# Optimization experiments

Measured on AMD Instinct MI355X. Metric: run time of the kernel, lower is better.

The kernel has to match this reference:

```python
import jax, jax.numpy as jnp
import numpy as np

B, N, H, IN, OUT = 2, 4096, 64, 32, 8


def setup_inputs() -> dict:
    key = jax.random.key(0)
    ks = jax.random.split(key, 18)
    sc = 0.1  # xavier-ish scale for H=64
    mask = lambda k: (jax.random.uniform(k, (1, N, N)) < 0.1).astype(jnp.float32)
    return {
        "x0": jax.random.normal(ks[0], (B, N, IN), jnp.float32),
        "h0": jax.random.normal(ks[1], (B, N, H), jnp.float32),
        "h1": jax.random.normal(ks[2], (B, N, H), jnp.float32),
        "h2": jax.random.normal(ks[3], (B, N, H), jnp.float32),
        "m00": mask(ks[4]), "m20": mask(ks[5]), "m01": mask(ks[6]),
        "m11": mask(ks[7]), "m12": mask(ks[8]), "m22": mask(ks[9]),
        "Wq": jax.random.normal(ks[10], (3, H, H), jnp.float32) * sc,
        "Wk": jax.random.normal(ks[11], (6, H, H), jnp.float32) * sc,
        "Wsu0": jax.random.normal(ks[12], (H, IN + H), jnp.float32) * sc,
        "Wsu12": jax.random.normal(ks[13], (2, H, H), jnp.float32) * sc,
        "Wdt": jax.random.normal(ks[14], (3, H, H), jnp.float32) * sc,
        "bdt": jnp.zeros((3, H), jnp.float32),
        "step_size": jnp.array(1.0, jnp.float32),
        "out_scale": jnp.array(10.0, jnp.float32),
    }


def _cosine_acc(q, keys_and_masks_and_vals):
    # q: [B,N,H]; each entry: (keys [B,Np,H], mask [1,N,Np], vals [B,Np,H])
    qn = q / jnp.linalg.norm(q, axis=2, keepdims=True)
    acc = 0.0
    for k, m, v in keys_and_masks_and_vals:
        kn = k / jnp.linalg.norm(k, axis=2, keepdims=True)
        scale = 1.0 / jnp.sum(m, axis=2, keepdims=True)
        rel = scale * m * jnp.einsum("bnh,bmh->bnm", qn, kn)  # [B,N,Np]
        acc = acc + jnp.einsum("bnm,bmh->bnh", rel, v)
    return acc


def reference(x0, h0, h1, h2, m00, m20, m01, m11, m12, m22,
              Wq, Wk, Wsu0, Wsu12, Wdt, bdt, step_size, out_scale):
    # queries per successor type, keys per edge; edges (pred->succ):
    # 0->0 (k0), 2->0 (k1), 0->1 (k2), 1->1 (k3), 1->2 (k4), 2->2 (k5)
    q0 = h0 @ Wq[0].T
    q1 = h1 @ Wq[1].T
    q2 = h2 @ Wq[2].T
    acc0 = _cosine_acc(q0, [(h0 @ Wk[0].T, m00, h0), (h2 @ Wk[1].T, m20, h2)])
    acc1 = _cosine_acc(q1, [(h0 @ Wk[2].T, m01, h0), (h1 @ Wk[3].T, m11, h1)])
    acc2 = _cosine_acc(q2, [(h1 @ Wk[4].T, m12, h1), (h2 @ Wk[5].T, m22, h2)])

    def step(h, acc_in, Wsu, t):
        dt = 2.0 * jax.nn.sigmoid(h @ Wdt[t].T + bdt[t]) - 1.0
        return h + step_size * dt * (acc_in @ Wsu.T)

    h0n = step(h0, jnp.concatenate([x0, acc0], axis=2), Wsu0, 0)
    h1n = step(h1, acc1, Wsu12[0], 1)
    h2n = step(h2, acc2, Wsu12[1], 2)
    out2 = out_scale * h2n[:, :, :OUT]
    return (out2, h0n, h1n, h2n)
```

## Files before the change

### kernel.cpp

```cpp
#include <hip/hip_runtime.h>

typedef __bf16 bf16;
typedef bf16 bf16x8 __attribute__((ext_vector_type(8)));
typedef float f32x4 __attribute__((ext_vector_type(4)));
typedef unsigned int uint;
typedef uint u32x4 __attribute__((ext_vector_type(4)));
typedef unsigned short u16x8 __attribute__((ext_vector_type(8)));

constexpr int NT = 4096;

__device__ __forceinline__ bf16x8 ld8f(const float* p) {
    f32x4 a = *(const f32x4*)p;
    f32x4 b = *(const f32x4*)(p + 4);
    bf16x8 v;
    v[0] = (bf16)a[0]; v[1] = (bf16)a[1]; v[2] = (bf16)a[2]; v[3] = (bf16)a[3];
    v[4] = (bf16)b[0]; v[5] = (bf16)b[1]; v[6] = (bf16)b[2]; v[7] = (bf16)b[3];
    return v;
}

__device__ __forceinline__ uint pack2(float a, float b) {
    unsigned short ua = __builtin_bit_cast(unsigned short, (bf16)a);
    unsigned short ub = __builtin_bit_cast(unsigned short, (bf16)b);
    return (uint)ua | ((uint)ub << 16);
}

__global__ __launch_bounds__(256) void prep_kernel(
    const float* __restrict__ h0, const float* __restrict__ h1, const float* __restrict__ h2,
    const float* __restrict__ Wq, const float* __restrict__ Wk,
    bf16* __restrict__ qn, bf16* __restrict__ kn, bf16* __restrict__ vT)
{
    __shared__ __align__(16) unsigned short tlds[4][16][72];
    const int tid = threadIdx.x, wid = tid >> 6, lane = tid & 63;
    const int l15 = lane & 15, quad = lane >> 4;
    const int bx = blockIdx.x;
    const int rt = bx & 127, sl = bx >> 7;
    const int g0 = rt * 64;
    const int grow = g0 + wid * 16 + l15;
    const float* hs[3] = {h0, h1, h2};

    bf16x8 af[3][2];
#pragma unroll
    for (int p = 0; p < 3; p++)
#pragma unroll
        for (int hc = 0; hc < 2; hc++)
            af[p][hc] = ld8f(hs[p] + (size_t)grow * 64 + hc * 32 + quad * 8);

    if (sl == 0) {
        const int gr0 = g0 + wid * 16;
        const int bb = gr0 >> 12, n0 = gr0 & 4095;
#pragma unroll
        for (int p = 0; p < 3; p++) {
#pragma unroll
            for (int hc = 0; hc < 2; hc++)
                *(u16x8*)(&tlds[wid][l15][hc * 32 + quad * 8]) = __builtin_bit_cast(u16x8, af[p][hc]);
            unsigned short vals[16];
#pragma unroll
            for (int r = 0; r < 16; r++) vals[r] = tlds[wid][r][lane];
            uint us[8];
#pragma unroll
            for (int k = 0; k < 8; k++) us[k] = (uint)vals[2 * k] | ((uint)vals[2 * k + 1] << 16);
            uint* dst = (uint*)(vT + ((size_t)(p * 2 + bb) * 64 + lane) * NT + n0);
            u32x4 w0 = {us[0], us[1], us[2], us[3]};
            u32x4 w1 = {us[4], us[5], us[6], us[7]};
            *(u32x4*)dst = w0;
            *(u32x4*)(dst + 4) = w1;
        }
    }

    const int predmap[6] = {0, 2, 0, 1, 1, 2};
    const int pj0 = sl * 3;
#pragma unroll
    for (int pi = 0; pi < 3; pi++) {
        const int pj = pj0 + pi;
        const float* W = (pj < 3) ? (Wq + pj * 4096) : (Wk + (pj - 3) * 4096);
        const int src = (pj < 3) ? pj : predmap[pj - 3];
        bf16* outp = (pj < 3) ? (qn + (size_t)pj * 2 * NT * 64)
                              : (kn + (size_t)(pj - 3) * 2 * NT * 64);
        f32x4 s[4];
#pragma unroll
        for (int it = 0; it < 4; it++) {
            f32x4 acc = {0.f, 0.f, 0.f, 0.f};
#pragma unroll
            for (int hc = 0; hc < 2; hc++) {
                bf16x8 wb = ld8f(W + (size_t)(it * 16 + l15) * 64 + hc * 32 + quad * 8);
                acc = __builtin_amdgcn_mfma_f32_16x16x32_bf16(af[src][hc], wb, acc, 0, 0, 0);
            }
            s[it] = acc;
        }
#pragma unroll
        for (int r = 0; r < 4; r++) {
            float ss = s[0][r] * s[0][r] + s[1][r] * s[1][r] + s[2][r] * s[2][r] + s[3][r] * s[3][r];
            ss += __shfl_xor(ss, 1); ss += __shfl_xor(ss, 2);
            ss += __shfl_xor(ss, 4); ss += __shfl_xor(ss, 8);
            float rn = rsqrtf(ss);
            s[0][r] *= rn; s[1][r] *= rn; s[2][r] *= rn; s[3][r] *= rn;
        }
        const int rowbase = g0 + wid * 16 + quad * 4;
#pragma unroll
        for (int it = 0; it < 4; it++)
#pragma unroll
            for (int r = 0; r < 4; r++)
                outp[(size_t)(rowbase + r) * 64 + it * 16 + l15] = (bf16)s[it][r];
    }
}

template<int JC>
__global__ __launch_bounds__(256, 3) void attn_kernel(
    const bf16* __restrict__ qn, const bf16* __restrict__ kn, const bf16* __restrict__ vT,
    const float* __restrict__ m00, const float* __restrict__ m20, const float* __restrict__ m01,
    const float* __restrict__ m11, const float* __restrict__ m12, const float* __restrict__ m22,
    float* __restrict__ Pacc, float* __restrict__ rsO)
{
    __shared__ __align__(16) bf16 Klds[2][64][72];
    __shared__ __align__(16) bf16 Vlds[2][64][72];
    const int tid = threadIdx.x, wid = tid >> 6, lane = tid & 63;
    const int l15 = lane & 15, quad = lane >> 4;
    const int bx = blockIdx.x;
    const int e = bx / (32 * JC);
    const int rem = bx % (32 * JC);
    const int qt = rem / JC, jcv = rem % JC;
    const int qrow0 = qt * 128, wstrip = wid * 32;
    const int qtypemap[6] = {0, 0, 1, 1, 2, 2};
    const int predmap[6]  = {0, 2, 0, 1, 1, 2};
    const float* masks[6] = {m00, m20, m01, m11, m12, m22};
    const float* __restrict__ mask = masks[e];
    const int qtv = qtypemap[e], pv = predmap[e];
    constexpr int JSPAN = NT / JC;
    constexpr int NI = JSPAN / 64;
    const int jbeg = jcv * JSPAN;

    int s_b[4], s_jl[4], s_ch[4];
#pragma unroll
    for (int i = 0; i < 4; i++) {
        int u = tid + 256 * i;
        s_b[i] = u >> 9; s_jl[i] = (u >> 3) & 63; s_ch[i] = u & 7;
    }

    bf16x8 Qf[2][2][2];
#pragma unroll
    for (int b = 0; b < 2; b++)
#pragma unroll
        for (int mt = 0; mt < 2; mt++)
#pragma unroll
            for (int hc = 0; hc < 2; hc++)
                Qf[b][mt][hc] = *(const bf16x8*)(qn +
                    ((size_t)(qtv * 2 + b) * NT + qrow0 + wstrip + mt * 16 + l15) * 64 +
                    hc * 32 + quad * 8);

    f32x4 acc2[2][4][2];
#pragma unroll
    for (int b = 0; b < 2; b++)
#pragma unroll
        for (int ht = 0; ht < 4; ht++)
#pragma unroll
            for (int mt = 0; mt < 2; mt++) {
                f32x4 z = {0.f, 0.f, 0.f, 0.f};
                acc2[b][ht][mt] = z;
            }
    float rsl[2] = {0.f, 0.f};

    u32x4 kreg[4], vreg[4];
#pragma unroll
    for (int i = 0; i < 4; i++) {
        kreg[i] = *(const u32x4*)(kn + ((size_t)(e * 2 + s_b[i]) * NT + jbeg + s_jl[i]) * 64 + s_ch[i] * 8);
        vreg[i] = *(const u32x4*)(vT + ((size_t)(pv * 2 + s_b[i]) * 64 + s_jl[i]) * NT + jbeg + s_ch[i] * 8);
    }
    f32x4 mv[2][4];
#pragma unroll
    for (int mt = 0; mt < 2; mt++)
#pragma unroll
        for (int jt = 0; jt < 4; jt++)
            mv[mt][jt] = *(const f32x4*)(mask +
                (size_t)(qrow0 + wstrip + mt * 16 + l15) * NT + jbeg + jt * 16 + quad * 4);

#pragma unroll 1
    for (int ji = 0; ji < NI; ji++) {
        const int jn = (ji + 1 < NI) ? (jbeg + (ji + 1) * 64) : jbeg;

        __syncthreads();
#pragma unroll
        for (int i = 0; i < 4; i++) {
            *(u32x4*)(&Klds[s_b[i]][s_jl[i]][s_ch[i] * 8]) = kreg[i];
            *(u32x4*)(&Vlds[s_b[i]][s_jl[i]][s_ch[i] * 8]) = vreg[i];
        }
        __syncthreads();

#pragma unroll
        for (int i = 0; i < 4; i++) {
            kreg[i] = *(const u32x4*)(kn + ((size_t)(e * 2 + s_b[i]) * NT + jn + s_jl[i]) * 64 + s_ch[i] * 8);
            vreg[i] = *(const u32x4*)(vT + ((size_t)(pv * 2 + s_b[i]) * 64 + s_jl[i]) * NT + jn + s_ch[i] * 8);
        }

#pragma unroll
        for (int mt = 0; mt < 2; mt++)
#pragma unroll
            for (int jt = 0; jt < 4; jt++)
                rsl[mt] += mv[mt][jt][0] + mv[mt][jt][1] + mv[mt][jt][2] + mv[mt][jt][3];

        uint Pd[2][4][2][2];
#pragma unroll
        for (int jt = 0; jt < 4; jt++)
#pragma unroll
            for (int b = 0; b < 2; b++)
#pragma unroll
                for (int mt = 0; mt < 2; mt++) {
                    f32x4 sc = {0.f, 0.f, 0.f, 0.f};
#pragma unroll
                    for (int hc = 0; hc < 2; hc++) {
                        bf16x8 a = *(const bf16x8*)(&Klds[b][jt * 16 + l15][hc * 32 + quad * 8]);
                        sc = __builtin_amdgcn_mfma_f32_16x16x32_bf16(a, Qf[b][mt][hc], sc, 0, 0, 0);
                    }
                    sc[0] *= mv[mt][jt][0]; sc[1] *= mv[mt][jt][1];
                    sc[2] *= mv[mt][jt][2]; sc[3] *= mv[mt][jt][3];
                    Pd[b][jt][mt][0] = pack2(sc[0], sc[1]);
                    Pd[b][jt][mt][1] = pack2(sc[2], sc[3]);
                }

#pragma unroll
        for (int mt = 0; mt < 2; mt++)
#pragma unroll
            for (int jt = 0; jt < 4; jt++)
                mv[mt][jt] = *(const f32x4*)(mask +
                    (size_t)(qrow0 + wstrip + mt * 16 + l15) * NT + jn + jt * 16 + quad * 4);

#pragma unroll
        for (int b = 0; b < 2; b++) {
            uint Bf[2][2][4];
#pragma unroll
            for (int mt = 0; mt < 2; mt++)
#pragma unroll
                for (int c = 0; c < 2; c++)
#pragma unroll
                    for (int v = 0; v < 4; v++) {
                        int srclane = ((((quad & 1) * 2 + (v >> 1)) * 16 + l15) << 2);
                        int lo = __builtin_amdgcn_ds_bpermute(srclane, (int)Pd[b][2 * c][mt][v & 1]);
                        int hi = __builtin_amdgcn_ds_bpermute(srclane, (int)Pd[b][2 * c + 1][mt][v & 1]);
                        Bf[mt][c][v] = (quad & 2) ? (uint)hi : (uint)lo;
                    }
#pragma unroll
            for (int ht = 0; ht < 4; ht++)
#pragma unroll
                for (int c = 0; c < 2; c++) {
                    bf16x8 a = *(const bf16x8*)(&Vlds[b][ht * 16 + l15][c * 32 + quad * 8]);
#pragma unroll
                    for (int mt = 0; mt < 2; mt++) {
                        u32x4 t = {Bf[mt][c][0], Bf[mt][c][1], Bf[mt][c][2], Bf[mt][c][3]};
                        bf16x8 bbv = __builtin_bit_cast(bf16x8, t);
                        acc2[b][ht][mt] =
                            __builtin_amdgcn_mfma_f32_16x16x32_bf16(a, bbv, acc2[b][ht][mt], 0, 0, 0);
                    }
                }
        }
    }

#pragma unroll
    for (int b = 0; b < 2; b++)
#pragma unroll
        for (int ht = 0; ht < 4; ht++)
#pragma unroll
            for (int mt = 0; mt < 2; mt++) {
                const int n = qrow0 + wstrip + mt * 16 + l15;
#pragma unroll
                for (int r = 0; r < 4; r++) {
                    const int h = ht * 16 + quad * 4 + r;
                    Pacc[(((size_t)(jcv * 6 + e) * 2 + b) * 64 + h) * NT + n] = acc2[b][ht][mt][r];
                }
            }
#pragma unroll
    for (int mt = 0; mt < 2; mt++) {
        float v = rsl[mt];
        v += __shfl_xor(v, 16);
        v += __shfl_xor(v, 32);
        if (quad == 0)
            rsO[(size_t)(jcv * 6 + e) * NT + qrow0 + wstrip + mt * 16 + l15] = v;
    }
}

template<int JC>
__global__ __launch_bounds__(256) void update_kernel(
    const float* __restrict__ x0, const float* __restrict__ h0,
    const float* __restrict__ h1, const float* __restrict__ h2,
    const float* __restrict__ Wsu0, const float* __restrict__ Wsu12,
    const float* __restrict__ Wdt, const float* __restrict__ bdt,
    const float* __restrict__ stepp, const float* __restrict__ oscp,
    const float* __restrict__ Pacc, const float* __restrict__ rs,
    float* __restrict__ dout)
{
    const int tid = threadIdx.x, wid = tid >> 6, lane = tid & 63;
    const int l15 = lane & 15, quad = lane >> 4;
    const int bx = blockIdx.x;
    const int rt = bx & 127, t = bx >> 7;
    const int g0 = rt * 64;
    const int grow = g0 + wid * 16 + l15;
    const int n = grow & 4095, bb = grow >> 12;
    const float step = *stepp, osc = *oscp;
    const float* hs[3] = {h0, h1, h2};
    const float* __restrict__ ht_base = hs[t];

    bf16x8 afh[2], afacc[2], afx;
#pragma unroll
    for (int hc = 0; hc < 2; hc++)
        afh[hc] = ld8f(ht_base + (size_t)grow * 64 + hc * 32 + quad * 8);
    if (t == 0) afx = ld8f(x0 + (size_t)grow * 32 + quad * 8);

    float s0 = 0.f, s1 = 0.f;
#pragma unroll
    for (int jc = 0; jc < JC; jc++) {
        s0 += rs[(size_t)(jc * 6 + 2 * t) * NT + n];
        s1 += rs[(size_t)(jc * 6 + 2 * t + 1) * NT + n];
    }
    const float i0 = 1.f / s0, i1 = 1.f / s1;
#pragma unroll
    for (int hc = 0; hc < 2; hc++) {
        float S0[8] = {0,0,0,0,0,0,0,0}, S1[8] = {0,0,0,0,0,0,0,0};
#pragma unroll
        for (int jc = 0; jc < JC; jc++) {
            const float* b0 = Pacc + (((size_t)(jc * 6 + 2 * t) * 2 + bb) * 64) * NT + n;
            const float* b1 = Pacc + (((size_t)(jc * 6 + 2 * t + 1) * 2 + bb) * 64) * NT + n;
#pragma unroll
            for (int j = 0; j < 8; j++) {
                const int h = hc * 32 + quad * 8 + j;
                S0[j] += b0[(size_t)h * NT];
                S1[j] += b1[(size_t)h * NT];
            }
        }
        bf16x8 v;
#pragma unroll
        for (int j = 0; j < 8; j++) v[j] = (bf16)(S0[j] * i0 + S1[j] * i1);
        afacc[hc] = v;
    }

    float bdtv[4];
#pragma unroll
    for (int it = 0; it < 4; it++)
        bdtv[it] = bdt[t * 64 + it * 16 + l15];

#pragma unroll
    for (int it = 0; it < 4; it++) {
        f32x4 z = {0.f, 0.f, 0.f, 0.f};
        f32x4 u = {0.f, 0.f, 0.f, 0.f};
#pragma unroll
        for (int hc = 0; hc < 2; hc++) {
            bf16x8 wb = ld8f(Wdt + (size_t)t * 4096 + (size_t)(it * 16 + l15) * 64 + hc * 32 + quad * 8);
            z = __builtin_amdgcn_mfma_f32_16x16x32_bf16(afh[hc], wb, z, 0, 0, 0);
        }
        if (t == 0) {
            bf16x8 w0 = ld8f(Wsu0 + (size_t)(it * 16 + l15) * 96 + quad * 8);
            u = __builtin_amdgcn_mfma_f32_16x16x32_bf16(afx, w0, u, 0, 0, 0);
#pragma unroll
            for (int kc = 0; kc < 2; kc++) {
                bf16x8 wk = ld8f(Wsu0 + (size_t)(it * 16 + l15) * 96 + 32 + kc * 32 + quad * 8);
                u = __builtin_amdgcn_mfma_f32_16x16x32_bf16(afacc[kc], wk, u, 0, 0, 0);
            }
        } else {
#pragma unroll
            for (int kc = 0; kc < 2; kc++) {
                bf16x8 wk = ld8f(Wsu12 + (size_t)(t - 1) * 4096 + (size_t)(it * 16 + l15) * 64 + kc * 32 + quad * 8);
                u = __builtin_amdgcn_mfma_f32_16x16x32_bf16(afacc[kc], wk, u, 0, 0, 0);
            }
        }
        const int colg = it * 16 + l15;
#pragma unroll
        for (int r = 0; r < 4; r++) {
            int row = g0 + wid * 16 + quad * 4 + r;
            float zz = z[r] + bdtv[it];
            float dtv = 2.f / (1.f + __expf(-zz)) - 1.f;
            float hval = ht_base[(size_t)row * 64 + colg];
            float hn = hval + step * dtv * u[r];
            dout[65536 + (size_t)t * 524288 + (size_t)row * 64 + colg] = hn;
            if (t == 2 && colg < 8)
                dout[(size_t)row * 8 + colg] = osc * hn;
        }
    }
}

extern "C" void kernel_launch(void* const* d_in, const int* in_sizes, int n_in,
                              void* d_out, int out_size, void* d_ws, size_t ws_size,
                              hipStream_t stream) {
    const float* x0   = (const float*)d_in[0];
    const float* h0   = (const float*)d_in[1];
    const float* h1   = (const float*)d_in[2];
    const float* h2   = (const float*)d_in[3];
    const float* m00  = (const float*)d_in[4];
    const float* m20  = (const float*)d_in[5];
    const float* m01  = (const float*)d_in[6];
    const float* m11  = (const float*)d_in[7];
    const float* m12  = (const float*)d_in[8];
    const float* m22  = (const float*)d_in[9];
    const float* Wq   = (const float*)d_in[10];
    const float* Wk   = (const float*)d_in[11];
    const float* Wsu0 = (const float*)d_in[12];
    const float* Wsu12= (const float*)d_in[13];
    const float* Wdt  = (const float*)d_in[14];
    const float* bdt  = (const float*)d_in[15];
    const float* step = (const float*)d_in[16];
    const float* oscl = (const float*)d_in[17];

    bf16* qn  = (bf16*)d_ws;
    bf16* kn  = qn + 1572864;
    bf16* vT  = kn + 3145728;
    float* Pacc = (float*)(vT + 1572864);

    auto need = [](size_t jc) { return 12582912 + jc * 12582912 + jc * 98304; };
    const int JC = (ws_size >= need(4)) ? 4 : ((ws_size >= need(2)) ? 2 : 1);

    prep_kernel<<<384, 256, 0, stream>>>(h0, h1, h2, Wq, Wk, qn, kn, vT);

    if (JC == 4) {
        float* rs = Pacc + (size_t)4 * 3145728;
        attn_kernel<4><<<6 * 32 * 4, 256, 0, stream>>>(qn, kn, vT, m00, m20, m01, m11, m12, m22, Pacc, rs);
        update_kernel<4><<<384, 256, 0, stream>>>(x0, h0, h1, h2, Wsu0, Wsu12, Wdt, bdt,
                                                  step, oscl, Pacc, rs, (float*)d_out);
    } else if (JC == 2) {
        float* rs = Pacc + (size_t)2 * 3145728;
        attn_kernel<2><<<6 * 32 * 2, 256, 0, stream>>>(qn, kn, vT, m00, m20, m01, m11, m12, m22, Pacc, rs);
        update_kernel<2><<<384, 256, 0, stream>>>(x0, h0, h1, h2, Wsu0, Wsu12, Wdt, bdt,
                                                  step, oscl, Pacc, rs, (float*)d_out);
    } else {
        float* rs = Pacc + (size_t)1 * 3145728;
        attn_kernel<1><<<6 * 32 * 1, 256, 0, stream>>>(qn, kn, vT, m00, m20, m01, m11, m12, m22, Pacc, rs);
        update_kernel<1><<<384, 256, 0, stream>>>(x0, h0, h1, h2, Wsu0, Wsu12, Wdt, bdt,
                                                  step, oscl, Pacc, rs, (float*)d_out);
    }
}
```

Baseline: 492.9 us.

## Split prep work across more blocks, use permlane swaps, transpose Pacc layout

The prep kernel now launches 1536 blocks, each computing one projection or one V transpose, where before each block handled three. In the attention kernel, K fragments are hoisted out of the mt loop, and the ds_bpermute shuffles are replaced with v_permlane32/16_swap instructions. The Pacc partial-sum layout changes from h-major to row-major with contiguous h, so the attention kernel stores f32x4 vectors and the update kernel reads them with vector loads instead of strided scalar accesses. Together these aim to cut LDS permute traffic and uncoalesced global accesses, at the cost of relying on the permlane lane semantics being correct.

After: 461.6 us. -6.4%, faster.

```diff
diff --git a/kernel.cpp b/kernel.cpp
--- a/kernel.cpp
+++ b/kernel.cpp
@@ -37,71 +37,68 @@
     const int g0 = rt * 64;
     const int grow = g0 + wid * 16 + l15;
     const float* hs[3] = {h0, h1, h2};
-
-    bf16x8 af[3][2];
-#pragma unroll
-    for (int p = 0; p < 3; p++)
+    const int predmap[6] = {0, 2, 0, 1, 1, 2};
+
+    if (sl >= 9) {
+        const int p = sl - 9;
+        bf16x8 af[2];
 #pragma unroll
         for (int hc = 0; hc < 2; hc++)
-            af[p][hc] = ld8f(hs[p] + (size_t)grow * 64 + hc * 32 + quad * 8);
-
-    if (sl == 0) {
+            af[hc] = ld8f(hs[p] + (size_t)grow * 64 + hc * 32 + quad * 8);
+#pragma unroll
+        for (int hc = 0; hc < 2; hc++)
+            *(u16x8*)(&tlds[wid][l15][hc * 32 + quad * 8]) = __builtin_bit_cast(u16x8, af[hc]);
+        unsigned short vals[16];
+#pragma unroll
+        for (int r = 0; r < 16; r++) vals[r] = tlds[wid][r][lane];
+        uint us[8];
+#pragma unroll
+        for (int k = 0; k < 8; k++) us[k] = (uint)vals[2 * k] | ((uint)vals[2 * k + 1] << 16);
         const int gr0 = g0 + wid * 16;
         const int bb = gr0 >> 12, n0 = gr0 & 4095;
-#pragma unroll
-        for (int p = 0; p < 3; p++) {
-#pragma unroll
-            for (int hc = 0; hc < 2; hc++)
-                *(u16x8*)(&tlds[wid][l15][hc * 32 + quad * 8]) = __builtin_bit_cast(u16x8, af[p][hc]);
-            unsigned short vals[16];
-#pragma unroll
-            for (int r = 0; r < 16; r++) vals[r] = tlds[wid][r][lane];
-            uint us[8];
-#pragma unroll
-            for (int k = 0; k < 8; k++) us[k] = (uint)vals[2 * k] | ((uint)vals[2 * k + 1] << 16);
-            uint* dst = (uint*)(vT + ((size_t)(p * 2 + bb) * 64 + lane) * NT + n0);
-            u32x4 w0 = {us[0], us[1], us[2], us[3]};
-            u32x4 w1 = {us[4], us[5], us[6], us[7]};
-            *(u32x4*)dst = w0;
-            *(u32x4*)(dst + 4) = w1;
-        }
-    }
-
-    const int predmap[6] = {0, 2, 0, 1, 1, 2};
-    const int pj0 = sl * 3;
-#pragma unroll
-    for (int pi = 0; pi < 3; pi++) {
-        const int pj = pj0 + pi;
-        const float* W = (pj < 3) ? (Wq + pj * 4096) : (Wk + (pj - 3) * 4096);
-        const int src = (pj < 3) ? pj : predmap[pj - 3];
-        bf16* outp = (pj < 3) ? (qn + (size_t)pj * 2 * NT * 64)
-                              : (kn + (size_t)(pj - 3) * 2 * NT * 64);
-        f32x4 s[4];
-#pragma unroll
-        for (int it = 0; it < 4; it++) {
-            f32x4 acc = {0.f, 0.f, 0.f, 0.f};
-#pragma unroll
-            for (int hc = 0; hc < 2; hc++) {
-                bf16x8 wb = ld8f(W + (size_t)(it * 16 + l15) * 64 + hc * 32 + quad * 8);
-                acc = __builtin_amdgcn_mfma_f32_16x16x32_bf16(af[src][hc], wb, acc, 0, 0, 0);
-            }
-            s[it] = acc;
-        }
-#pragma unroll
-        for (int r = 0; r < 4; r++) {
-            float ss = s[0][r] * s[0][r] + s[1][r] * s[1][r] + s[2][r] * s[2][r] + s[3][r] * s[3][r];
-            ss += __shfl_xor(ss, 1); ss += __shfl_xor(ss, 2);
-            ss += __shfl_xor(ss, 4); ss += __shfl_xor(ss, 8);
-            float rn = rsqrtf(ss);
-            s[0][r] *= rn; s[1][r] *= rn; s[2][r] *= rn; s[3][r] *= rn;
-        }
-        const int rowbase = g0 + wid * 16 + quad * 4;
-#pragma unroll
-        for (int it = 0; it < 4; it++)
-#pragma unroll
-            for (int r = 0; r < 4; r++)
-                outp[(size_t)(rowbase + r) * 64 + it * 16 + l15] = (bf16)s[it][r];
-    }
+        uint* dst = (uint*)(vT + ((size_t)(p * 2 + bb) * 64 + lane) * NT + n0);
+        u32x4 w0 = {us[0], us[1], us[2], us[3]};
+        u32x4 w1 = {us[4], us[5], us[6], us[7]};
+        *(u32x4*)dst = w0;
+        *(u32x4*)(dst + 4) = w1;
+        return;
+    }
+
+    const int pj = sl;
+    const float* W = (pj < 3) ? (Wq + pj * 4096) : (Wk + (pj - 3) * 4096);
+    const int src = (pj < 3) ? pj : predmap[pj - 3];
+    bf16* outp = (pj < 3) ? (qn + (size_t)pj * 2 * NT * 64)
+                          : (kn + (size_t)(pj - 3) * 2 * NT * 64);
+    bf16x8 af[2];
+#pragma unroll
+    for (int hc = 0; hc < 2; hc++)
+        af[hc] = ld8f(hs[src] + (size_t)grow * 64 + hc * 32 + quad * 8);
+
+    f32x4 s[4];
+#pragma unroll
+    for (int it = 0; it < 4; it++) {
+        f32x4 acc = {0.f, 0.f, 0.f, 0.f};
+#pragma unroll
+        for (int hc = 0; hc < 2; hc++) {
+            bf16x8 wb = ld8f(W + (size_t)(it * 16 + l15) * 64 + hc * 32 + quad * 8);
+            acc = __builtin_amdgcn_mfma_f32_16x16x32_bf16(af[hc], wb, acc, 0, 0, 0);
+        }
+        s[it] = acc;
+    }
+#pragma unroll
+    for (int r = 0; r < 4; r++) {
+        float ss = s[0][r] * s[0][r] + s[1][r] * s[1][r] + s[2][r] * s[2][r] + s[3][r] * s[3][r];
+        ss += __shfl_xor(ss, 1); ss += __shfl_xor(ss, 2);
+        ss += __shfl_xor(ss, 4); ss += __shfl_xor(ss, 8);
+        float rn = rsqrtf(ss);
+        s[0][r] *= rn; s[1][r] *= rn; s[2][r] *= rn; s[3][r] *= rn;
+    }
+    const int rowbase = g0 + wid * 16 + quad * 4;
+#pragma unroll
+    for (int it = 0; it < 4; it++)
+#pragma unroll
+        for (int r = 0; r < 4; r++)
+            outp[(size_t)(rowbase + r) * 64 + it * 16 + l15] = (bf16)s[it][r];
 }
 
 template<int JC>
@@ -201,20 +198,20 @@
 #pragma unroll
         for (int jt = 0; jt < 4; jt++)
 #pragma unroll
-            for (int b = 0; b < 2; b++)
+            for (int b = 0; b < 2; b++) {
+                bf16x8 aK0 = *(const bf16x8*)(&Klds[b][jt * 16 + l15][quad * 8]);
+                bf16x8 aK1 = *(const bf16x8*)(&Klds[b][jt * 16 + l15][32 + quad * 8]);
 #pragma unroll
                 for (int mt = 0; mt < 2; mt++) {
                     f32x4 sc = {0.f, 0.f, 0.f, 0.f};
-#pragma unroll
-                    for (int hc = 0; hc < 2; hc++) {
-                        bf16x8 a = *(const bf16x8*)(&Klds[b][jt * 16 + l15][hc * 32 + quad * 8]);
-                        sc = __builtin_amdgcn_mfma_f32_16x16x32_bf16(a, Qf[b][mt][hc], sc, 0, 0, 0);
-                    }
+                    sc = __builtin_amdgcn_mfma_f32_16x16x32_bf16(aK0, Qf[b][mt][0], sc, 0, 0, 0);
+                    sc = __builtin_amdgcn_mfma_f32_16x16x32_bf16(aK1, Qf[b][mt][1], sc, 0, 0, 0);
                     sc[0] *= mv[mt][jt][0]; sc[1] *= mv[mt][jt][1];
                     sc[2] *= mv[mt][jt][2]; sc[3] *= mv[mt][jt][3];
                     Pd[b][jt][mt][0] = pack2(sc[0], sc[1]);
                     Pd[b][jt][mt][1] = pack2(sc[2], sc[3]);
                 }
+            }
 
 #pragma unroll
         for (int mt = 0; mt < 2; mt++)
@@ -231,11 +228,14 @@
 #pragma unroll
                 for (int c = 0; c < 2; c++)
 #pragma unroll
-                    for (int v = 0; v < 4; v++) {
-                        int srclane = ((((quad & 1) * 2 + (v >> 1)) * 16 + l15) << 2);
-                        int lo = __builtin_amdgcn_ds_bpermute(srclane, (int)Pd[b][2 * c][mt][v & 1]);
-                        int hi = __builtin_amdgcn_ds_bpermute(srclane, (int)Pd[b][2 * c + 1][mt][v & 1]);
-                        Bf[mt][c][v] = (quad & 2) ? (uint)hi : (uint)lo;
+                    for (int d = 0; d < 2; d++) {
+                        uint x = Pd[b][2 * c][mt][d];
+                        uint y = Pd[b][2 * c + 1][mt][d];
+                        asm("v_permlane32_swap_b32 %0, %1\n\t"
+                            "v_permlane16_swap_b32 %0, %1"
+                            : "+v"(x), "+v"(y));
+                        Bf[mt][c][d]     = x;
+                        Bf[mt][c][d + 2] = y;
                     }
 #pragma unroll
             for (int ht = 0; ht < 4; ht++)
@@ -260,11 +260,8 @@
 #pragma unroll
             for (int mt = 0; mt < 2; mt++) {
                 const int n = qrow0 + wstrip + mt * 16 + l15;
-#pragma unroll
-                for (int r = 0; r < 4; r++) {
-                    const int h = ht * 16 + quad * 4 + r;
-                    Pacc[(((size_t)(jcv * 6 + e) * 2 + b) * 64 + h) * NT + n] = acc2[b][ht][mt][r];
-                }
+                *(f32x4*)(Pacc + ((((size_t)(jcv * 6 + e) * 2 + b) * NT + n) << 6) +
+                          ht * 16 + quad * 4) = acc2[b][ht][mt];
             }
 #pragma unroll
     for (int mt = 0; mt < 2; mt++) {
@@ -312,21 +309,22 @@
     const float i0 = 1.f / s0, i1 = 1.f / s1;
 #pragma unroll
     for (int hc = 0; hc < 2; hc++) {
-        float S0[8] = {0,0,0,0,0,0,0,0}, S1[8] = {0,0,0,0,0,0,0,0};
+        f32x4 S0a = {0.f,0.f,0.f,0.f}, S0b = {0.f,0.f,0.f,0.f};
+        f32x4 S1a = {0.f,0.f,0.f,0.f}, S1b = {0.f,0.f,0.f,0.f};
 #pragma unroll
         for (int jc = 0; jc < JC; jc++) {
-            const float* b0 = Pacc + (((size_t)(jc * 6 + 2 * t) * 2 + bb) * 64) * NT + n;
-            const float* b1 = Pacc + (((size_t)(jc * 6 + 2 * t + 1) * 2 + bb) * 64) * NT + n;
-#pragma unroll
-            for (int j = 0; j < 8; j++) {
-                const int h = hc * 32 + quad * 8 + j;
-                S0[j] += b0[(size_t)h * NT];
-                S1[j] += b1[(size_t)h * NT];
-            }
+            const float* p0 = Pacc + ((((size_t)(jc * 6 + 2 * t) * 2 + bb) * NT + n) << 6) +
+                              hc * 32 + quad * 8;
+            const float* p1 = Pacc + ((((size_t)(jc * 6 + 2 * t + 1) * 2 + bb) * NT + n) << 6) +
+                              hc * 32 + quad * 8;
+            S0a += *(const f32x4*)p0;  S0b += *(const f32x4*)(p0 + 4);
+            S1a += *(const f32x4*)p1;  S1b += *(const f32x4*)(p1 + 4);
         }
         bf16x8 v;
 #pragma unroll
-        for (int j = 0; j < 8; j++) v[j] = (bf16)(S0[j] * i0 + S1[j] * i1);
+        for (int j = 0; j < 4; j++) v[j]     = (bf16)(S0a[j] * i0 + S1a[j] * i1);
+#pragma unroll
+        for (int j = 0; j < 4; j++) v[4 + j] = (bf16)(S0b[j] * i0 + S1b[j] * i1);
         afacc[hc] = v;
     }
 
@@ -404,7 +402,7 @@
     auto need = [](size_t jc) { return 12582912 + jc * 12582912 + jc * 98304; };
     const int JC = (ws_size >= need(4)) ? 4 : ((ws_size >= need(2)) ? 2 : 1);
 
-    prep_kernel<<<384, 256, 0, stream>>>(h0, h1, h2, Wq, Wk, qn, kn, vT);
+    prep_kernel<<<1536, 256, 0, stream>>>(h0, h1, h2, Wq, Wk, qn, kn, vT);
 
     if (JC == 4) {
         float* rs = Pacc + (size_t)4 * 3145728;
```
